# Kernel optimization log

Hardware: AMD Instinct MI355X
Metric: run time of the kernel (lower is better)

## Reference

```python
import jax, jax.numpy as jnp
import numpy as np
from jax import lax

VOCAB = 35095 + 2
WORD_DIM = 300
MAX_SENT = 3000
N_FILT = 100
N_CLASSES = 10


def setup_inputs() -> dict:
    key = jax.random.key(0)
    ks = jax.random.split(key, 10)
    x = jax.random.randint(ks[0], (2, MAX_SENT), 0, VOCAB)
    emb = jax.random.normal(ks[1], (VOCAB, WORD_DIM), dtype=jnp.float32) * 0.1
    emb = emb.at[0].set(0.0)  # padding_idx=0
    w1 = jax.random.normal(ks[2], (N_FILT, 1, 3), dtype=jnp.float32) * 0.1
    b1 = jax.random.normal(ks[3], (N_FILT,), dtype=jnp.float32) * 0.01
    w2 = jax.random.normal(ks[4], (N_FILT, 1, 4), dtype=jnp.float32) * 0.1
    b2 = jax.random.normal(ks[5], (N_FILT,), dtype=jnp.float32) * 0.01
    w3 = jax.random.normal(ks[6], (N_FILT, 1, 5), dtype=jnp.float32) * 0.1
    b3 = jax.random.normal(ks[7], (N_FILT,), dtype=jnp.float32) * 0.01
    fc_w = jax.random.normal(ks[8], (N_CLASSES, 3 * N_FILT), dtype=jnp.float32) * 0.05
    fc_b = jax.random.normal(ks[9], (N_CLASSES,), dtype=jnp.float32) * 0.01
    return {"x": x, "emb": emb, "w1": w1, "b1": b1, "w2": w2, "b2": b2,
            "w3": w3, "b3": b3, "fc_w": fc_w, "fc_b": fc_b}


def _conv_relu_maxpool(h, w, b):
    # h: [B, 1, L]; w: [F, 1, K]  ->  [B, F]
    y = lax.conv_general_dilated(h, w, window_strides=(1,), padding='VALID',
                                 dimension_numbers=('NCW', 'OIW', 'NCW'))
    y = jnp.maximum(y + b[None, :, None], 0.0)
    return jnp.max(y, axis=2)


def reference(x, emb, w1, b1, w2, b2, w3, b3, fc_w, fc_b):
    # Embedding lookup then flatten to a single-channel 1D signal of length 900k
    h = emb[x].reshape(-1, 1, WORD_DIM * MAX_SENT)  # [B, 1, 900000]
    c1 = _conv_relu_maxpool(h, w1, b1)  # [B, 100]
    c2 = _conv_relu_maxpool(h, w2, b2)
    c3 = _conv_relu_maxpool(h, w3, b3)
    feats = jnp.concatenate([c1, c2, c3], axis=1)  # [B, 300]
    # Dropout is identity at inference
    return feats @ fc_w.T + fc_b
```

## Files before the change

kernel.cpp:

```cpp
#include <hip/hip_runtime.h>

#define VOCAB   35097
#define DDIM    300
#define NWORDS  3000
#define L_SIG   900000
#define NFILT   100
#define NCLS    10

#define QQ      28
#define WIN     (QQ + 4)
#define BLK_POS (64 * QQ)
#define NBLKA   503
#define FPG     5
#define NGRPW   5

__device__ __forceinline__ float relu_(float v) { return fmaxf(v, 0.0f); }

template<bool TAIL>
__device__ __forceinline__ void run_group(
    const float (&h)[WIN], int t0, int f0, int lane,
    const float* __restrict__ w1, const float* __restrict__ w2,
    const float* __restrict__ w3,
    float* __restrict__ pslot)
{
  int n3 = QQ, n4 = QQ, n5 = QQ;
  if (TAIL) {
    n3 = min(max(899998 - t0, 0), QQ);
    n4 = min(max(899997 - t0, 0), QQ);
    n5 = min(max(899996 - t0, 0), QQ);
  }
  const float NEG = -__builtin_huge_valf();

  float a3[FPG], a4[FPG], a5[FPG];

  #pragma unroll
  for (int j = 0; j < FPG; ++j) {
    const int fu = __builtin_amdgcn_readfirstlane(f0 + j);
    const float a0 = w1[fu*3+0], a1 = w1[fu*3+1], a2 = w1[fu*3+2];
    const float c0 = w2[fu*4+0], c1 = w2[fu*4+1], c2 = w2[fu*4+2], c3 = w2[fu*4+3];
    const float e0 = w3[fu*5+0], e1 = w3[fu*5+1], e2 = w3[fu*5+2], e3 = w3[fu*5+3], e4 = w3[fu*5+4];

    float m3a = NEG, m3b = NEG, m4a = NEG, m4b = NEG, m5a = NEG, m5b = NEG;

    if (!TAIL) {
      #pragma unroll
      for (int p = 0; p < QQ; p += 2) {
        float v3a = fmaf(a0, h[p],   fmaf(a1, h[p+1], a2 * h[p+2]));
        float v3b = fmaf(a0, h[p+1], fmaf(a1, h[p+2], a2 * h[p+3]));
        if (((p >> 1) & 1) == 0) m3a = fmaxf(fmaxf(m3a, v3a), v3b);
        else                     m3b = fmaxf(fmaxf(m3b, v3a), v3b);
        float v4a = fmaf(c0, h[p],   fmaf(c1, h[p+1], fmaf(c2, h[p+2], c3 * h[p+3])));
        float v4b = fmaf(c0, h[p+1], fmaf(c1, h[p+2], fmaf(c2, h[p+3], c3 * h[p+4])));
        if (((p >> 1) & 1) == 0) m4a = fmaxf(fmaxf(m4a, v4a), v4b);
        else                     m4b = fmaxf(fmaxf(m4b, v4a), v4b);
        float v5a = fmaf(e0, h[p],   fmaf(e1, h[p+1], fmaf(e2, h[p+2], fmaf(e3, h[p+3], e4 * h[p+4]))));
        float v5b = fmaf(e0, h[p+1], fmaf(e1, h[p+2], fmaf(e2, h[p+3], fmaf(e3, h[p+4], e4 * h[p+5]))));
        if (((p >> 1) & 1) == 0) m5a = fmaxf(fmaxf(m5a, v5a), v5b);
        else                     m5b = fmaxf(fmaxf(m5b, v5a), v5b);
      }
    } else {
      #pragma unroll
      for (int p = 0; p < QQ; ++p) {
        float v3 = fmaf(a0, h[p], fmaf(a1, h[p+1], a2 * h[p+2]));
        float v4 = fmaf(c0, h[p], fmaf(c1, h[p+1], fmaf(c2, h[p+2], c3 * h[p+3])));
        float v5 = fmaf(e0, h[p], fmaf(e1, h[p+1], fmaf(e2, h[p+2], fmaf(e3, h[p+3], e4 * h[p+4]))));
        if (p < n3) { if (p & 1) m3b = fmaxf(m3b, v3); else m3a = fmaxf(m3a, v3); }
        if (p < n4) { if (p & 1) m4b = fmaxf(m4b, v4); else m4a = fmaxf(m4a, v4); }
        if (p < n5) { if (p & 1) m5b = fmaxf(m5b, v5); else m5a = fmaxf(m5a, v5); }
      }
    }
    a3[j] = fmaxf(m3a, m3b);
    a4[j] = fmaxf(m4a, m4b);
    a5[j] = fmaxf(m5a, m5b);
  }

  #pragma unroll
  for (int s = 1; s < 64; s <<= 1) {
    #pragma unroll
    for (int j = 0; j < FPG; ++j) {
      a3[j] = fmaxf(a3[j], __shfl_xor(a3[j], s));
      a4[j] = fmaxf(a4[j], __shfl_xor(a4[j], s));
      a5[j] = fmaxf(a5[j], __shfl_xor(a5[j], s));
    }
  }

  if (lane == 0) {
    #pragma unroll
    for (int j = 0; j < FPG; ++j) {
      pslot[j]      = a3[j];
      pslot[5 + j]  = a4[j];
      pslot[10 + j] = a5[j];
    }
  }
}

__global__ __launch_bounds__(256, 4) void conv_max_kernel(
    const int* __restrict__ x, const float* __restrict__ emb,
    const float* __restrict__ w1, const float* __restrict__ w2,
    const float* __restrict__ w3,
    float* __restrict__ partial)
{
  const int lane  = threadIdx.x & 63;
  const int wave  = threadIdx.x >> 6;
  const int batch = blockIdx.y;
  const int t0_blk = blockIdx.x * BLK_POS;
  const int t0     = t0_blk + lane * QQ;
  const int fbase  = wave * (FPG * NGRPW);

  float h[WIN];
  {
    int w0 = t0 / DDIM;
    int d0 = t0 - w0 * DDIM;
    int wa = min(w0, NWORDS - 1);
    int wb = min(w0 + 1, NWORDS - 1);
    int xa = x[batch * NWORDS + wa];
    int xb = x[batch * NWORDS + wb];
    const float4* rowA = (const float4*)(emb + (size_t)xa * DDIM) + (d0 >> 2);
    const float4* rowB = (const float4*)(emb + (size_t)xb * DDIM);
    const int nf4 = (DDIM - d0) >> 2;
    #pragma unroll
    for (int i = 0; i < WIN / 4; ++i) {
      const float4* src = (i < nf4) ? (rowA + i) : (rowB + (i - nf4));
      float4 v = *src;
      h[4*i+0] = v.x; h[4*i+1] = v.y; h[4*i+2] = v.z; h[4*i+3] = v.w;
    }
  }

  float* pwave = partial + ((size_t)batch * NBLKA + blockIdx.x) * 300 + wave * (FPG * 3 * NGRPW / NGRPW) * NGRPW;
  pwave = partial + ((size_t)batch * NBLKA + blockIdx.x) * 300 + wave * 75;

  const bool tail = (t0_blk + BLK_POS + 4) > L_SIG;
  if (tail) {
    #pragma unroll 1
    for (int g = 0; g < NGRPW; ++g)
      run_group<true >(h, t0, fbase + g * FPG, lane, w1, w2, w3, pwave + g * 15);
  } else {
    #pragma unroll 1
    for (int g = 0; g < NGRPW; ++g)
      run_group<false>(h, t0, fbase + g * FPG, lane, w1, w2, w3, pwave + g * 15);
  }
}

__global__ void reduce_kernel(const float* __restrict__ partial,
                              const float* __restrict__ b1,
                              const float* __restrict__ b2,
                              const float* __restrict__ b3,
                              float* __restrict__ feats)
{
  const int p    = blockIdx.x;
  const int b    = threadIdx.x >> 6;
  const int lane = threadIdx.x & 63;

  const int wv = p / 75, r = p % 75, g = r / 15, q = r % 15;
  const int conv = q / 5, j = q % 5;
  const int f = wv * 25 + g * 5 + j;

  const float* col = partial + (size_t)b * NBLKA * 300 + p;
  float m = -__builtin_huge_valf();
  for (int i = lane; i < NBLKA; i += 64)
    m = fmaxf(m, col[(size_t)i * 300]);
  #pragma unroll
  for (int s = 1; s < 64; s <<= 1)
    m = fmaxf(m, __shfl_xor(m, s));

  if (lane == 0) {
    const float bias = (conv == 0) ? b1[f] : (conv == 1) ? b2[f] : b3[f];
    feats[b * 300 + conv * NFILT + f] = relu_(m + bias);
  }
}

__global__ void fc_kernel(const float* __restrict__ feats,
                          const float* __restrict__ fcw,
                          const float* __restrict__ fcb,
                          float* __restrict__ out)
{
  const int b = blockIdx.x / NCLS;
  const int c = blockIdx.x % NCLS;
  const int lane = threadIdx.x;
  float s = 0.0f;
  for (int k = lane; k < 3 * NFILT; k += 64)
    s += feats[b * 3 * NFILT + k] * fcw[c * 3 * NFILT + k];
  #pragma unroll
  for (int k = 1; k < 64; k <<= 1) s += __shfl_xor(s, k);
  if (lane == 0) out[b * NCLS + c] = s + fcb[c];
}

extern "C" void kernel_launch(void* const* d_in, const int* in_sizes, int n_in,
                              void* d_out, int out_size, void* d_ws, size_t ws_size,
                              hipStream_t stream)
{
  const int*   x   = (const int*)  d_in[0];
  const float* emb = (const float*)d_in[1];
  const float* w1  = (const float*)d_in[2];
  const float* b1  = (const float*)d_in[3];
  const float* w2  = (const float*)d_in[4];
  const float* b2  = (const float*)d_in[5];
  const float* w3  = (const float*)d_in[6];
  const float* b3  = (const float*)d_in[7];
  const float* fcw = (const float*)d_in[8];
  const float* fcb = (const float*)d_in[9];
  float* out = (float*)d_out;

  float* partial = (float*)d_ws;
  float* feats   = partial + (size_t)2 * NBLKA * 300;

  dim3 grid(NBLKA, 2);
  conv_max_kernel<<<grid, 256, 0, stream>>>(x, emb, w1, w2, w3, partial);
  reduce_kernel<<<300, 128, 0, stream>>>(partial, b1, b2, b3, feats);
  fc_kernel<<<2 * NCLS, 64, 0, stream>>>(feats, fcw, fcb, out);
}
```

Baseline: 181.1 us.

## Use packed FP32 FMA for conv windows and transpose partial-max layout

Rewrites the non-tail conv inner loop to use v_pk_fma_f32/v_pk_mul_f32 on pairs of positions (first and second half of each lane's window), so one instruction handles two output positions. The per-block partial maxima are now stored transposed (filter-major, padded to 512 blocks), so the reduce kernel reads contiguous rows with one 64-thread block per (batch, filter). The packed path needs extra registers for the paired copies of the window, and inline asm may limit compiler scheduling.

New measurement: 171.2 us. 1.06x faster.

```diff
diff --git a/kernel.cpp b/kernel.cpp
--- a/kernel.cpp
+++ b/kernel.cpp
@@ -8,17 +8,34 @@
 #define NCLS    10
 
 #define QQ      28
+#define HALF    14
 #define WIN     (QQ + 4)
+#define NHP     (HALF + 4)
 #define BLK_POS (64 * QQ)
 #define NBLKA   503
+#define NBLKP   512
 #define FPG     5
 #define NGRPW   5
 
+typedef __attribute__((ext_vector_type(2))) float f32x2;
+
 __device__ __forceinline__ float relu_(float v) { return fmaxf(v, 0.0f); }
+
+__device__ __forceinline__ f32x2 pk_mul(f32x2 a, f32x2 b) {
+  f32x2 d;
+  asm("v_pk_mul_f32 %0, %1, %2" : "=v"(d) : "v"(a), "v"(b));
+  return d;
+}
+__device__ __forceinline__ f32x2 pk_fma(f32x2 a, f32x2 b, f32x2 c) {
+  f32x2 d;
+  asm("v_pk_fma_f32 %0, %1, %2, %3" : "=v"(d) : "v"(a), "v"(b), "v"(c));
+  return d;
+}
+__device__ __forceinline__ f32x2 dup2(float w) { f32x2 d; d.x = w; d.y = w; return d; }
 
 template<bool TAIL>
 __device__ __forceinline__ void run_group(
-    const float (&h)[WIN], int t0, int f0, int lane,
+    const float (&h)[WIN], const f32x2 (&hp)[NHP], int t0, int f0, int lane,
     const float* __restrict__ w1, const float* __restrict__ w2,
     const float* __restrict__ w3,
     float* __restrict__ pslot)
@@ -43,20 +60,33 @@
     float m3a = NEG, m3b = NEG, m4a = NEG, m4b = NEG, m5a = NEG, m5b = NEG;
 
     if (!TAIL) {
+      const f32x2 pa0 = dup2(a0), pa1 = dup2(a1), pa2 = dup2(a2);
+      const f32x2 pc0 = dup2(c0), pc1 = dup2(c1), pc2 = dup2(c2), pc3 = dup2(c3);
+      const f32x2 pe0 = dup2(e0), pe1 = dup2(e1), pe2 = dup2(e2), pe3 = dup2(e3), pe4 = dup2(e4);
+
       #pragma unroll
-      for (int p = 0; p < QQ; p += 2) {
-        float v3a = fmaf(a0, h[p],   fmaf(a1, h[p+1], a2 * h[p+2]));
-        float v3b = fmaf(a0, h[p+1], fmaf(a1, h[p+2], a2 * h[p+3]));
-        if (((p >> 1) & 1) == 0) m3a = fmaxf(fmaxf(m3a, v3a), v3b);
-        else                     m3b = fmaxf(fmaxf(m3b, v3a), v3b);
-        float v4a = fmaf(c0, h[p],   fmaf(c1, h[p+1], fmaf(c2, h[p+2], c3 * h[p+3])));
-        float v4b = fmaf(c0, h[p+1], fmaf(c1, h[p+2], fmaf(c2, h[p+3], c3 * h[p+4])));
-        if (((p >> 1) & 1) == 0) m4a = fmaxf(fmaxf(m4a, v4a), v4b);
-        else                     m4b = fmaxf(fmaxf(m4b, v4a), v4b);
-        float v5a = fmaf(e0, h[p],   fmaf(e1, h[p+1], fmaf(e2, h[p+2], fmaf(e3, h[p+3], e4 * h[p+4]))));
-        float v5b = fmaf(e0, h[p+1], fmaf(e1, h[p+2], fmaf(e2, h[p+3], fmaf(e3, h[p+4], e4 * h[p+5]))));
-        if (((p >> 1) & 1) == 0) m5a = fmaxf(fmaxf(m5a, v5a), v5b);
-        else                     m5b = fmaxf(fmaxf(m5b, v5a), v5b);
+      for (int p = 0; p < HALF; ++p) {
+        f32x2 t3 = pk_mul(pa2, hp[p+2]);
+        t3 = pk_fma(pa1, hp[p+1], t3);
+        t3 = pk_fma(pa0, hp[p+0], t3);
+        f32x2 t4 = pk_mul(pc3, hp[p+3]);
+        t4 = pk_fma(pc2, hp[p+2], t4);
+        t4 = pk_fma(pc1, hp[p+1], t4);
+        t4 = pk_fma(pc0, hp[p+0], t4);
+        f32x2 t5 = pk_mul(pe4, hp[p+4]);
+        t5 = pk_fma(pe3, hp[p+3], t5);
+        t5 = pk_fma(pe2, hp[p+2], t5);
+        t5 = pk_fma(pe1, hp[p+1], t5);
+        t5 = pk_fma(pe0, hp[p+0], t5);
+        if (p & 1) {
+          m3b = fmaxf(fmaxf(m3b, t3.x), t3.y);
+          m4b = fmaxf(fmaxf(m4b, t4.x), t4.y);
+          m5b = fmaxf(fmaxf(m5b, t5.x), t5.y);
+        } else {
+          m3a = fmaxf(fmaxf(m3a, t3.x), t3.y);
+          m4a = fmaxf(fmaxf(m4a, t4.x), t4.y);
+          m5a = fmaxf(fmaxf(m5a, t5.x), t5.y);
+        }
       }
     } else {
       #pragma unroll
@@ -87,9 +117,9 @@
   if (lane == 0) {
     #pragma unroll
     for (int j = 0; j < FPG; ++j) {
-      pslot[j]      = a3[j];
-      pslot[5 + j]  = a4[j];
-      pslot[10 + j] = a5[j];
+      pslot[(size_t)(j)      * NBLKP] = a3[j];
+      pslot[(size_t)(5 + j)  * NBLKP] = a4[j];
+      pslot[(size_t)(10 + j) * NBLKP] = a5[j];
     }
   }
 }
@@ -126,18 +156,23 @@
     }
   }
 
-  float* pwave = partial + ((size_t)batch * NBLKA + blockIdx.x) * 300 + wave * (FPG * 3 * NGRPW / NGRPW) * NGRPW;
-  pwave = partial + ((size_t)batch * NBLKA + blockIdx.x) * 300 + wave * 75;
+  f32x2 hp[NHP];
+  #pragma unroll
+  for (int k = 0; k < NHP; ++k) { f32x2 t; t.x = h[k]; t.y = h[k + HALF]; hp[k] = t; }
+
+  float* prow = partial + ((size_t)batch * 300 + wave * 75) * NBLKP + blockIdx.x;
 
   const bool tail = (t0_blk + BLK_POS + 4) > L_SIG;
   if (tail) {
     #pragma unroll 1
     for (int g = 0; g < NGRPW; ++g)
-      run_group<true >(h, t0, fbase + g * FPG, lane, w1, w2, w3, pwave + g * 15);
+      run_group<true >(h, hp, t0, fbase + g * FPG, lane, w1, w2, w3,
+                       prow + (size_t)g * 15 * NBLKP);
   } else {
     #pragma unroll 1
     for (int g = 0; g < NGRPW; ++g)
-      run_group<false>(h, t0, fbase + g * FPG, lane, w1, w2, w3, pwave + g * 15);
+      run_group<false>(h, hp, t0, fbase + g * FPG, lane, w1, w2, w3,
+                       prow + (size_t)g * 15 * NBLKP);
   }
 }
 
@@ -147,18 +182,19 @@
                               const float* __restrict__ b3,
                               float* __restrict__ feats)
 {
-  const int p    = blockIdx.x;
-  const int b    = threadIdx.x >> 6;
-  const int lane = threadIdx.x & 63;
+  const int idx  = blockIdx.x;
+  const int b    = idx / 300;
+  const int p    = idx % 300;
+  const int lane = threadIdx.x;
 
   const int wv = p / 75, r = p % 75, g = r / 15, q = r % 15;
   const int conv = q / 5, j = q % 5;
   const int f = wv * 25 + g * 5 + j;
 
-  const float* col = partial + (size_t)b * NBLKA * 300 + p;
+  const float* row = partial + ((size_t)b * 300 + p) * NBLKP;
   float m = -__builtin_huge_valf();
   for (int i = lane; i < NBLKA; i += 64)
-    m = fmaxf(m, col[(size_t)i * 300]);
+    m = fmaxf(m, row[i]);
   #pragma unroll
   for (int s = 1; s < 64; s <<= 1)
     m = fmaxf(m, __shfl_xor(m, s));
@@ -202,10 +238,10 @@
   float* out = (float*)d_out;
 
   float* partial = (float*)d_ws;
-  float* feats   = partial + (size_t)2 * NBLKA * 300;
+  float* feats   = partial + (size_t)2 * 300 * NBLKP;
 
   dim3 grid(NBLKA, 2);
   conv_max_kernel<<<grid, 256, 0, stream>>>(x, emb, w1, w2, w3, partial);
-  reduce_kernel<<<300, 128, 0, stream>>>(partial, b1, b2, b3, feats);
+  reduce_kernel<<<600, 64, 0, stream>>>(partial, b1, b2, b3, feats);
   fc_kernel<<<2 * NCLS, 64, 0, stream>>>(feats, fcw, fcb, out);
 }
```
